# Kernel tuning notes

Measured on AMD Instinct MI355X. Metric: run time of the kernel, lower is better.

Reference implementation:

```python
import jax, jax.numpy as jnp
import numpy as np

E = 512      # embed_size
H = 8        # heads
HD = E // H  # head_dim
TN = 288     # time_num
FE = 4       # forward_expansion
N, T = 64, 512


def layernorm(x, g, b, eps=1e-5):
    mu = jnp.mean(x, axis=-1, keepdims=True)
    var = jnp.mean((x - mu) ** 2, axis=-1, keepdims=True)
    return (x - mu) * jax.lax.rsqrt(var + eps) * g + b


def setup_inputs() -> dict:
    key = jax.random.key(0)
    ks = jax.random.split(key, 12)
    w = lambda k, sh: jax.random.normal(k, sh, dtype=jnp.float32) * 0.02
    return {
        "value": jax.random.normal(ks[0], (N, T, E), dtype=jnp.float32),
        "key_in": jax.random.normal(ks[1], (N, T, E), dtype=jnp.float32),
        "query": jax.random.normal(ks[2], (N, T, E), dtype=jnp.float32),
        "i": 37,
        # One_hot_encoder params: learned identity-init table + linear to embed
        "I_mat": jnp.eye(TN, dtype=jnp.float32),
        "oh_W": w(ks[3], (TN, E)), "oh_b": jnp.zeros((E,), jnp.float32),
        # per-head projections (shared across heads, as in the torch module)
        "Wv": w(ks[4], (HD, HD)), "Wk": w(ks[5], (HD, HD)), "Wq": w(ks[6], (HD, HD)),
        "Wo": w(ks[7], (E, E)), "bo": jnp.zeros((E,), jnp.float32),
        "g1": jnp.ones((E,), jnp.float32), "b1": jnp.zeros((E,), jnp.float32),
        "g2": jnp.ones((E,), jnp.float32), "b2": jnp.zeros((E,), jnp.float32),
        "W1": w(ks[8], (E, FE * E)), "bf1": jnp.zeros((FE * E,), jnp.float32),
        "W2": w(ks[9], (FE * E, E)), "bf2": jnp.zeros((E,), jnp.float32),
    }


def reference(value, key_in, query, i, I_mat, oh_W, oh_b, Wv, Wk, Wq, Wo, bo,
              g1, b1, g2, b2, W1, bf1, W2, bf2):
    n, t, c = query.shape
    # One_hot_encoder: rows i..i+T-1 (mod time_num) of learned table -> linear
    rows = (i + jnp.arange(t)) % TN
    onehot = I_mat[rows] @ oh_W + oh_b            # (T, E), broadcast over N
    q_in = query + onehot[None, :, :]
    # per-head projections
    v = value.reshape(n, t, H, HD) @ Wv           # (N,T,H,HD)
    k = key_in.reshape(n, t, H, HD) @ Wk
    qh = q_in.reshape(n, t, H, HD) @ Wq
    # attention (note: scale uses sqrt(embed_size), per original code)
    energy = jnp.einsum("nqhd,nkhd->nhqk", qh, k) / jnp.sqrt(jnp.float32(E))
    attn = jax.nn.softmax(energy, axis=-1)
    out = jnp.einsum("nhqk,nkhd->nqhd", attn, v).reshape(n, t, E)
    out = out @ Wo + bo
    # residual + LN + FFN + residual + LN (dropout=0 -> identity)
    x = layernorm(out + q_in, g1, b1)
    ff = jax.nn.relu(x @ W1 + bf1) @ W2 + bf2
    return layernorm(ff + x, g2, b2)
```

## Files before the change

### kernel.cpp

```cpp
#include <hip/hip_runtime.h>

typedef __attribute__((ext_vector_type(8))) short s16x8;
typedef __attribute__((ext_vector_type(4))) float f32x4;

#define TN 288

__device__ __forceinline__ unsigned short f2bf(float f) {
  union { float f; unsigned u; } v; v.f = f;
  unsigned r = v.u + 0x7fffu + ((v.u >> 16) & 1u);
  return (unsigned short)(r >> 16);
}
__device__ __forceinline__ float bf2f(unsigned short u) {
  union { float f; unsigned u; } v; v.u = ((unsigned)u) << 16;
  return v.f;
}
__device__ __forceinline__ unsigned lds_addr(const void* p) {
  return (unsigned)(unsigned long long)(const __attribute__((address_space(3))) char*)p;
}
__device__ __forceinline__ void async_copy16(unsigned short* lds, const unsigned short* g) {
  __builtin_amdgcn_global_load_lds(
      (const __attribute__((address_space(1))) unsigned int*)g,
      (__attribute__((address_space(3))) unsigned int*)lds, 16, 0, 0);
}

__device__ __forceinline__ void pack_body(const float* __restrict__ W,
    unsigned short* __restrict__ out, int N, long t) {
  int lr = (int)(t & 15);
  int lg = (int)((t >> 4) & 3);
  long g6 = t >> 6;
  int nt = N >> 4;
  int n16 = (int)(g6 % nt);
  int kb = (int)(g6 / nt) << 5;
  int k = kb + lg * 8;
  int col = n16 * 16 + lr;
  s16x8 v;
#pragma unroll
  for (int j = 0; j < 8; ++j) v[j] = (short)f2bf(W[(size_t)(k + j) * N + col]);
  *(s16x8*)(out + t * 8) = v;
}

__global__ __launch_bounds__(256) void prep_kernel(const int* __restrict__ pi,
    const float* __restrict__ I_mat, const float* __restrict__ ohW,
    const float* __restrict__ ohb, float* __restrict__ onehot,
    const float* __restrict__ Wv, const float* __restrict__ Wk,
    const float* __restrict__ Wq, unsigned short* __restrict__ Wv_b,
    unsigned short* __restrict__ Wk_b, unsigned short* __restrict__ Wq_b,
    const float* __restrict__ Wo, const float* __restrict__ W1,
    const float* __restrict__ W2, unsigned short* __restrict__ Wop,
    unsigned short* __restrict__ W1p, unsigned short* __restrict__ W2p) {
  int b = blockIdx.x, tid = threadIdx.x;
  if (b < 512) {
    int t = b;
    int r = (pi[0] + t) % TN;
    float acc0 = ohb[tid], acc1 = ohb[tid + 256];
    const float* Ir = I_mat + (size_t)r * TN;
    for (int j = 0; j < TN; ++j) {
      float iv = Ir[j];
      acc0 += iv * ohW[(size_t)j * 512 + tid];
      acc1 += iv * ohW[(size_t)j * 512 + tid + 256];
    }
    onehot[(size_t)t * 512 + tid] = acc0;
    onehot[(size_t)t * 512 + tid + 256] = acc1;
  } else if (b < 640) {
    pack_body(Wo, Wop, 512, (long)(b - 512) * 256 + tid);
  } else if (b < 1152) {
    pack_body(W1, W1p, 2048, (long)(b - 640) * 256 + tid);
  } else if (b < 1664) {
    pack_body(W2, W2p, 512, (long)(b - 1152) * 256 + tid);
  } else {
    int which = b - 1664;
    const float* src = which == 0 ? Wv : (which == 1 ? Wk : Wq);
    unsigned short* dst = which == 0 ? Wv_b : (which == 1 ? Wk_b : Wq_b);
    float sc = which == 2 ? 0.06375871424f : 1.f;
#pragma unroll
    for (int j = 0; j < 4; ++j) {
      int i = tid * 16 + j * 4;
      float4 f = *(const float4*)(src + i);
      unsigned lo = (unsigned)f2bf(f.x * sc) | ((unsigned)f2bf(f.y * sc) << 16);
      unsigned hi = (unsigned)f2bf(f.z * sc) | ((unsigned)f2bf(f.w * sc) << 16);
      *(uint2*)(dst + i) = make_uint2(lo, hi);
    }
  }
}

__global__ __launch_bounds__(256) void proj_all(
    const float* __restrict__ value, const float* __restrict__ key_in,
    const float* __restrict__ query, const unsigned short* __restrict__ Wv_b,
    const unsigned short* __restrict__ Wk_b, const unsigned short* __restrict__ Wq_b,
    const float* __restrict__ onehot, unsigned short* __restrict__ vT,
    unsigned short* __restrict__ k_p, unsigned short* __restrict__ q_p) {
  __shared__ unsigned short As[64][40];
  __shared__ unsigned short Bs[64][40];
  __shared__ unsigned short Cs[64][72];
  const int which = blockIdx.x >> 12;
  const int mb = blockIdx.x & 4095;
  const float* A = which == 0 ? value : (which == 1 ? key_in : query);
  const unsigned short* B = which == 0 ? Wv_b : (which == 1 ? Wk_b : Wq_b);
  unsigned short* C = which == 0 ? vT : (which == 1 ? k_p : q_p);
  const bool qin = (which == 2);
  const int m0 = mb * 64;
  const int tid = threadIdx.x, w = tid >> 6, l = tid & 63, lr = l & 15, lg = l >> 4;
  const int wr = (w >> 1) * 32, wc = (w & 1) * 32;
  const int aRow = (tid * 8) >> 5, aK = (tid * 8) & 31;
  const int bK = (tid * 8) >> 6, bCol = (tid * 8) & 63;
  f32x4 acc[2][2] = {};
  for (int kb = 0; kb < 64; kb += 32) {
    size_t fl = (size_t)(m0 + aRow) * 64 + kb + aK;
    float4 f0 = *(const float4*)(A + fl);
    float4 f1 = *(const float4*)(A + fl + 4);
    if (qin) {
      const float* oh = onehot + (fl & 262143);
      float4 o0 = *(const float4*)(oh);
      float4 o1 = *(const float4*)(oh + 4);
      f0.x += o0.x; f0.y += o0.y; f0.z += o0.z; f0.w += o0.w;
      f1.x += o1.x; f1.y += o1.y; f1.z += o1.z; f1.w += o1.w;
    }
    s16x8 av;
    av[0] = (short)f2bf(f0.x); av[1] = (short)f2bf(f0.y);
    av[2] = (short)f2bf(f0.z); av[3] = (short)f2bf(f0.w);
    av[4] = (short)f2bf(f1.x); av[5] = (short)f2bf(f1.y);
    av[6] = (short)f2bf(f1.z); av[7] = (short)f2bf(f1.w);
    *(s16x8*)&As[aRow][aK] = av;
    s16x8 bv = *(const s16x8*)(B + (size_t)(kb + bK) * 64 + bCol);
#pragma unroll
    for (int j = 0; j < 8; ++j) Bs[bCol + j][bK] = (unsigned short)bv[j];
    __syncthreads();
    s16x8 af0 = *(const s16x8*)&As[wr + lr][lg * 8];
    s16x8 af1 = *(const s16x8*)&As[wr + 16 + lr][lg * 8];
    s16x8 bf0 = *(const s16x8*)&Bs[wc + lr][lg * 8];
    s16x8 bf1 = *(const s16x8*)&Bs[wc + 16 + lr][lg * 8];
    acc[0][0] = __builtin_amdgcn_mfma_f32_16x16x32_bf16(af0, bf0, acc[0][0], 0, 0, 0);
    acc[0][1] = __builtin_amdgcn_mfma_f32_16x16x32_bf16(af0, bf1, acc[0][1], 0, 0, 0);
    acc[1][0] = __builtin_amdgcn_mfma_f32_16x16x32_bf16(af1, bf0, acc[1][0], 0, 0, 0);
    acc[1][1] = __builtin_amdgcn_mfma_f32_16x16x32_bf16(af1, bf1, acc[1][1], 0, 0, 0);
    __syncthreads();
  }
  if (which != 0) {
#pragma unroll
    for (int fi = 0; fi < 2; ++fi)
#pragma unroll
      for (int fj = 0; fj < 2; ++fj)
#pragma unroll
        for (int r = 0; r < 4; ++r) {
          int row = m0 + wr + fi * 16 + lg * 4 + r;
          int col = wc + fj * 16 + lr;
          C[(size_t)row * 64 + col] = f2bf(acc[fi][fj][r]);
        }
  } else {
#pragma unroll
    for (int fi = 0; fi < 2; ++fi)
#pragma unroll
      for (int fj = 0; fj < 2; ++fj)
#pragma unroll
        for (int r = 0; r < 4; ++r)
          Cs[wr + fi * 16 + lg * 4 + r][wc + fj * 16 + lr] = f2bf(acc[fi][fj][r]);
    __syncthreads();
    int nIdx = m0 >> 12, t0 = (m0 >> 3) & 511;
#pragma unroll
    for (int it = 0; it < 2; ++it) {
      int p = tid + it * 256;
      int hh = p >> 6, d = p & 63;
      s16x8 vv;
#pragma unroll
      for (int j = 0; j < 8; ++j) vv[j] = (short)Cs[j * 8 + hh][d];
      *(s16x8*)(C + (((size_t)(nIdx * 8 + hh) * 64 + d) << 9) + t0) = vv;
    }
  }
}

template<bool RELU, bool OUTBF, bool RES>
__global__ __launch_bounds__(256) void gemmF(
    const unsigned short* __restrict__ A, int lda,
    const unsigned short* __restrict__ Bp, int ldbp, int nOff,
    const float* __restrict__ bias, void* __restrict__ Cout,
    const unsigned short* __restrict__ resid, int ldc,
    int M, int K, int nby) {
  __shared__ unsigned short As[2][8192];
  const int tid = threadIdx.x, w = tid >> 6, l = tid & 63, lr = l & 15, lg = l >> 4;
  const int nwg = gridDim.x;
  const int bid = (blockIdx.x & 7) * (nwg >> 3) + (blockIdx.x >> 3);
  const int bx = bid / nby, by = bid % nby;
  const int m0 = bx * 128;
  const int wr = (w >> 1) * 64, wc = (w & 1) * 64;
  const int srow = tid >> 3, sc8 = tid & 7;
  const int gcol = (sc8 ^ (srow & 7)) * 8;
  const unsigned short* Ag = A + (size_t)(m0 + srow) * lda + gcol;
  const size_t ldaa = (size_t)32 * lda;
  const unsigned short* Bg = Bp +
      ((size_t)(nOff >> 4) + by * 8 + (wc >> 4)) * 512 + lg * 128 + lr * 8;
  const size_t bks = (size_t)ldbp * 512;

  f32x4 acc[4][4] = {};
  s16x8 b0[4], b1[4];

#pragma unroll
  for (int it = 0; it < 4; ++it)
    async_copy16(&As[0][(it * 256 + tid) * 8], Ag + it * ldaa);
#pragma unroll
  for (int fj = 0; fj < 4; ++fj) {
    b0[fj] = *(const s16x8*)(Bg + fj * 512);
    b1[fj] = *(const s16x8*)(Bg + bks + fj * 512);
  }
  __syncthreads();

  int buf = 0;
  for (int kb = 0; kb < K; kb += 64) {
    int kn = (kb + 64 < K) ? kb + 64 : 0;
#pragma unroll
    for (int it = 0; it < 4; ++it)
      async_copy16(&As[buf ^ 1][(it * 256 + tid) * 8], Ag + kn + it * ldaa);
    s16x8 b0n[4];
    {
      const unsigned short* p = Bg + ((size_t)(kn >> 5)) * bks;
#pragma unroll
      for (int fj = 0; fj < 4; ++fj) b0n[fj] = *(const s16x8*)(p + fj * 512);
    }
    {
      s16x8 af[4];
#pragma unroll
      for (int fi = 0; fi < 4; ++fi) {
        int row = wr + fi * 16 + lr;
        af[fi] = *(const s16x8*)&As[buf][row * 64 + ((lg ^ (row & 7)) * 8)];
      }
#pragma unroll
      for (int fi = 0; fi < 4; ++fi)
#pragma unroll
        for (int fj = 0; fj < 4; ++fj)
          acc[fi][fj] = __builtin_amdgcn_mfma_f32_16x16x32_bf16(af[fi], b0[fj], acc[fi][fj], 0, 0, 0);
    }
    s16x8 b1n[4];
    {
      const unsigned short* p = Bg + ((size_t)((kn + 32) >> 5)) * bks;
#pragma unroll
      for (int fj = 0; fj < 4; ++fj) b1n[fj] = *(const s16x8*)(p + fj * 512);
    }
    {
      s16x8 af[4];
#pragma unroll
      for (int fi = 0; fi < 4; ++fi) {
        int row = wr + fi * 16 + lr;
        af[fi] = *(const s16x8*)&As[buf][row * 64 + (((4 + lg) ^ (row & 7)) * 8)];
      }
#pragma unroll
      for (int fi = 0; fi < 4; ++fi)
#pragma unroll
        for (int fj = 0; fj < 4; ++fj)
          acc[fi][fj] = __builtin_amdgcn_mfma_f32_16x16x32_bf16(af[fi], b1[fj], acc[fi][fj], 0, 0, 0);
    }
    __syncthreads();
#pragma unroll
    for (int fj = 0; fj < 4; ++fj) { b0[fj] = b0n[fj]; b1[fj] = b1n[fj]; }
    buf ^= 1;
  }

#pragma unroll
  for (int fj = 0; fj < 4; ++fj) {
    int colL = by * 128 + wc + fj * 16 + lr;
    float bv = bias[nOff + colL];
#pragma unroll
    for (int fi = 0; fi < 4; ++fi)
#pragma unroll
      for (int r = 0; r < 4; ++r) {
        int row = m0 + wr + fi * 16 + lg * 4 + r;
        size_t ci = (size_t)row * ldc + colL;
        float v = acc[fi][fj][r] + bv;
        if (RES) v += bf2f(resid[ci]);
        if (RELU) v = fmaxf(v, 0.f);
        if (OUTBF) ((unsigned short*)Cout)[ci] = f2bf(v);
        else ((float*)Cout)[ci] = v;
      }
  }
}

__global__ __launch_bounds__(256, 2) void attn_kernel(
    const unsigned short* __restrict__ Qp, const unsigned short* __restrict__ Kp,
    const unsigned short* __restrict__ Vt, unsigned short* __restrict__ Out) {
  __shared__ unsigned short KS[128][72];
  __shared__ unsigned short P[4][16][132];
  const int bid = blockIdx.x;
  const int qh = bid >> 9, g = bid & 511, h = g & 7, n = g >> 3;
  const int tid = threadIdx.x, w = tid >> 6, l = tid & 63, lr = l & 15, lg = l >> 4;
  const int q0 = qh * 256;

  s16x8 qf[4][2];
#pragma unroll
  for (int rt = 0; rt < 4; ++rt) {
    const size_t qb = (((size_t)(n * 512 + q0 + w * 64 + rt * 16 + lr)) * 8 + h) * 64;
    qf[rt][0] = *(const s16x8*)(Qp + qb + lg * 8);
    qf[rt][1] = *(const s16x8*)(Qp + qb + 32 + lg * 8);
  }
  const unsigned short* Vb = Vt + ((size_t)(n * 8 + h)) * 32768 + (size_t)lr * 512 + lg * 8;

  f32x4 oacc[4][4] = {};
  float m[4][4], lsum[4][4];
#pragma unroll
  for (int rt = 0; rt < 4; ++rt)
#pragma unroll
    for (int r = 0; r < 4; ++r) { m[rt][r] = -1e30f; lsum[rt][r] = 0.f; }
  s16x8 vreg[16];

#pragma unroll
  for (int it = 0; it < 4; ++it) {
    int idx = tid + it * 256;
    int rr = idx >> 3, dd = (idx & 7) * 8;
    *(s16x8*)&KS[rr][dd] =
        *(const s16x8*)(Kp + (((size_t)(n * 512 + rr)) * 8 + h) * 64 + dd);
  }
#pragma unroll
  for (int ks = 0; ks < 4; ++ks)
#pragma unroll
    for (int fj = 0; fj < 4; ++fj)
      vreg[ks * 4 + fj] = *(const s16x8*)(Vb + fj * 8192 + ks * 32);
  __syncthreads();

  for (int c = 0; c < 4; ++c) {
    if (c) {
      __syncthreads();
#pragma unroll
      for (int it = 0; it < 4; ++it) {
        int idx = tid + it * 256;
        int rr = idx >> 3, dd = (idx & 7) * 8;
        *(s16x8*)&KS[rr][dd] =
            *(const s16x8*)(Kp + (((size_t)(n * 512 + c * 128 + rr)) * 8 + h) * 64 + dd);
      }
#pragma unroll
      for (int ks = 0; ks < 4; ++ks)
#pragma unroll
        for (int fj = 0; fj < 4; ++fj)
          vreg[ks * 4 + fj] = *(const s16x8*)(Vb + fj * 8192 + c * 128 + ks * 32);
      __syncthreads();
    }
#pragma unroll
    for (int rt = 0; rt < 4; ++rt) {
      f32x4 sacc[8];
      __builtin_amdgcn_s_setprio(1);
#pragma unroll
      for (int f = 0; f < 8; ++f) {
        s16x8 b0 = *(const s16x8*)&KS[f * 16 + lr][lg * 8];
        s16x8 b1 = *(const s16x8*)&KS[f * 16 + lr][32 + lg * 8];
        f32x4 a = {};
        a = __builtin_amdgcn_mfma_f32_16x16x32_bf16(qf[rt][0], b0, a, 0, 0, 0);
        a = __builtin_amdgcn_mfma_f32_16x16x32_bf16(qf[rt][1], b1, a, 0, 0, 0);
        sacc[f] = a;
      }
      __builtin_amdgcn_s_setprio(0);

      float fs[4];
#pragma unroll
      for (int r = 0; r < 4; ++r) {
        float cm = sacc[0][r];
#pragma unroll
        for (int f = 1; f < 8; ++f) cm = fmaxf(cm, sacc[f][r]);
#pragma unroll
        for (int mk = 1; mk < 16; mk <<= 1) cm = fmaxf(cm, __shfl_xor(cm, mk));
        float mn = fmaxf(m[rt][r], cm);
        fs[r] = __builtin_amdgcn_exp2f(m[rt][r] - mn);
        m[rt][r] = mn;
        unsigned pa = lds_addr(&P[w][lg * 4 + r][lr]);
        float cs = 0.f;
#pragma unroll
        for (int f = 0; f < 8; ++f) {
          float p = __builtin_amdgcn_exp2f(sacc[f][r] - mn);
          asm volatile("ds_write_b16_d16_hi %0, %1 offset:%2"
                       :: "v"(pa), "v"(p), "i"(f * 32) : "memory");
          cs += p;
        }
#pragma unroll
        for (int mk = 1; mk < 16; mk <<= 1) cs += __shfl_xor(cs, mk);
        lsum[rt][r] = lsum[rt][r] * fs[r] + cs;
      }
#pragma unroll
      for (int fj = 0; fj < 4; ++fj)
#pragma unroll
        for (int r = 0; r < 4; ++r) oacc[rt][fj][r] *= fs[r];

      asm volatile("s_waitcnt lgkmcnt(0)" ::: "memory");
      __builtin_amdgcn_sched_barrier(0);
      __builtin_amdgcn_s_setprio(1);
#pragma unroll
      for (int ks = 0; ks < 4; ++ks) {
        s16x8 pa = *(const s16x8*)&P[w][lr][ks * 32 + lg * 8];
#pragma unroll
        for (int fj = 0; fj < 4; ++fj)
          oacc[rt][fj] = __builtin_amdgcn_mfma_f32_16x16x32_bf16(pa, vreg[ks * 4 + fj], oacc[rt][fj], 0, 0, 0);
      }
      __builtin_amdgcn_s_setprio(0);
    }
  }

#pragma unroll
  for (int rt = 0; rt < 4; ++rt)
#pragma unroll
    for (int fj = 0; fj < 4; ++fj)
#pragma unroll
      for (int r = 0; r < 4; ++r) {
        int qrow = q0 + w * 64 + rt * 16 + lg * 4 + r;
        Out[((size_t)(n * 512 + qrow)) * 512 + h * 64 + fj * 16 + lr] =
            f2bf(oacc[rt][fj][r] / lsum[rt][r]);
      }
}

template<bool XBF, bool RES, bool RBF, bool QIN, bool OUTBF>
__global__ __launch_bounds__(256) void ln_kernel(const void* __restrict__ Xv,
    const void* __restrict__ Rv, const float* __restrict__ onehot,
    const float* __restrict__ g, const float* __restrict__ bb,
    void* __restrict__ outv) {
  int row = blockIdx.x * 4 + (threadIdx.x >> 6);
  int l = threadIdx.x & 63;
  size_t base = (size_t)row * 512 + l * 8;
  float v[8];
  if (XBF) {
    s16x8 xv = *(const s16x8*)((const unsigned short*)Xv + base);
#pragma unroll
    for (int j = 0; j < 8; ++j) v[j] = bf2f((unsigned short)xv[j]);
  } else {
    const float* X = (const float*)Xv;
    float4 x0 = *(const float4*)(X + base);
    float4 x1 = *(const float4*)(X + base + 4);
    v[0] = x0.x; v[1] = x0.y; v[2] = x0.z; v[3] = x0.w;
    v[4] = x1.x; v[5] = x1.y; v[6] = x1.z; v[7] = x1.w;
  }
  if (RES) {
    if (RBF) {
      s16x8 rv = *(const s16x8*)((const unsigned short*)Rv + base);
#pragma unroll
      for (int j = 0; j < 8; ++j) v[j] += bf2f((unsigned short)rv[j]);
    } else {
      const float* R = (const float*)Rv;
      float4 r0 = *(const float4*)(R + base);
      float4 r1 = *(const float4*)(R + base + 4);
      v[0] += r0.x; v[1] += r0.y; v[2] += r0.z; v[3] += r0.w;
      v[4] += r1.x; v[5] += r1.y; v[6] += r1.z; v[7] += r1.w;
    }
  }
  if (QIN) {
    size_t ob = (size_t)(row & 511) * 512 + l * 8;
    float4 o0 = *(const float4*)(onehot + ob);
    float4 o1 = *(const float4*)(onehot + ob + 4);
    v[0] += o0.x; v[1] += o0.y; v[2] += o0.z; v[3] += o0.w;
    v[4] += o1.x; v[5] += o1.y; v[6] += o1.z; v[7] += o1.w;
  }
  float s = 0.f, ss = 0.f;
#pragma unroll
  for (int j = 0; j < 8; ++j) { s += v[j]; ss += v[j] * v[j]; }
#pragma unroll
  for (int mk = 1; mk < 64; mk <<= 1) { s += __shfl_xor(s, mk); ss += __shfl_xor(ss, mk); }
  float mu = s * (1.f / 512.f);
  float inv = rsqrtf(ss * (1.f / 512.f) - mu * mu + 1e-5f);
#pragma unroll
  for (int j = 0; j < 8; ++j) {
    int e = l * 8 + j;
    float y = (v[j] - mu) * inv * g[e] + bb[e];
    if (OUTBF) ((unsigned short*)outv)[base + j] = f2bf(y);
    else ((float*)outv)[base + j] = y;
  }
}

extern "C" void kernel_launch(void* const* d_in, const int* in_sizes, int n_in,
                              void* d_out, int out_size, void* d_ws, size_t ws_size,
                              hipStream_t stream) {
  const float* value  = (const float*)d_in[0];
  const float* key_in = (const float*)d_in[1];
  const float* query  = (const float*)d_in[2];
  const int*   pi     = (const int*)d_in[3];
  const float* I_mat  = (const float*)d_in[4];
  const float* ohW    = (const float*)d_in[5];
  const float* ohb    = (const float*)d_in[6];
  const float* Wv     = (const float*)d_in[7];
  const float* Wk     = (const float*)d_in[8];
  const float* Wq     = (const float*)d_in[9];
  const float* Wo     = (const float*)d_in[10];
  const float* bo     = (const float*)d_in[11];
  const float* g1     = (const float*)d_in[12];
  const float* b1     = (const float*)d_in[13];
  const float* g2     = (const float*)d_in[14];
  const float* b2     = (const float*)d_in[15];
  const float* W1     = (const float*)d_in[16];
  const float* bf1    = (const float*)d_in[17];
  const float* W2     = (const float*)d_in[18];
  const float* bf2    = (const float*)d_in[19];

  char* ws = (char*)d_ws;
  const size_t MB = 1024 * 1024;
  unsigned short* q_p  = (unsigned short*)d_out;
  unsigned short* k_p  = q_p + 16777216;
  unsigned short* vT     = (unsigned short*)(ws + 0);
  unsigned short* attn_o = (unsigned short*)(ws + 32 * MB);
  unsigned short* x_b    = (unsigned short*)(ws + 64 * MB);
  unsigned short* ff1h   = (unsigned short*)(ws + 0);
  float*          onehot = (float*)(ws + 96 * MB);
  unsigned short* Wv_b   = (unsigned short*)(ws + 97 * MB);
  unsigned short* Wk_b   = Wv_b + 4096;
  unsigned short* Wq_b   = Wk_b + 4096;
  unsigned short* Wop    = Wq_b + 4096;
  unsigned short* W1p    = Wop + 262144;
  unsigned short* W2p    = W1p + 1048576;

  prep_kernel<<<1667, 256, 0, stream>>>(pi, I_mat, ohW, ohb, onehot,
      Wv, Wk, Wq, Wv_b, Wk_b, Wq_b, Wo, W1, W2, Wop, W1p, W2p);

  proj_all<<<12288, 256, 0, stream>>>(value, key_in, query,
      Wv_b, Wk_b, Wq_b, onehot, vT, k_p, q_p);

  attn_kernel<<<1024, 256, 0, stream>>>(q_p, k_p, vT, attn_o);

  gemmF<false, true, false><<<1024, 256, 0, stream>>>(
      attn_o, 512, Wop, 32, 0, bo, x_b, nullptr, 512, 32768, 512, 4);
  ln_kernel<true, true, false, true, true><<<8192, 256, 0, stream>>>(
      x_b, query, onehot, g1, b1, x_b);

  for (int hf = 0; hf < 2; ++hf) {
    const unsigned short* xh = x_b + (size_t)hf * 16384 * 512;
    gemmF<true, true, false><<<2048, 256, 0, stream>>>(
        xh, 512, W1p, 128, 0, bf1, ff1h, nullptr, 2048, 16384, 512, 16);
    gemmF<false, false, true><<<512, 256, 0, stream>>>(
        ff1h, 2048, W2p, 32, 0, bf2, (float*)d_out + (size_t)hf * 16384 * 512,
        xh, 512, 16384, 2048, 4);
  }
  ln_kernel<false, false, false, false, false><<<8192, 256, 0, stream>>>(
      d_out, nullptr, nullptr, g2, b2, d_out);
}
```

Measured before the change: 460.5 us.

## Pre-swizzle V into MFMA fragment layout and halve attention query tile

The V projection now writes its output in a layout that matches the MFMA B-fragment order, so each lane can read its fragment with one contiguous 16-byte load. The attention kernel stops keeping all V fragments in registers; it loads them from global memory inside the PV loop, which is now kept rolled. Each block handles 128 queries instead of 256 and the grid doubles to 2048 blocks, which lowers register pressure and may raise occupancy. The cost is that K chunks are loaded and staged by twice as many blocks, and the V loads now sit on the critical path of the PV MFMAs.

```diff
diff --git a/kernel.cpp b/kernel.cpp
--- a/kernel.cpp
+++ b/kernel.cpp
@@ -87,7 +87,7 @@
     const float* __restrict__ value, const float* __restrict__ key_in,
     const float* __restrict__ query, const unsigned short* __restrict__ Wv_b,
     const unsigned short* __restrict__ Wk_b, const unsigned short* __restrict__ Wq_b,
-    const float* __restrict__ onehot, unsigned short* __restrict__ vT,
+    const float* __restrict__ onehot, unsigned short* __restrict__ vP,
     unsigned short* __restrict__ k_p, unsigned short* __restrict__ q_p) {
   __shared__ unsigned short As[64][40];
   __shared__ unsigned short Bs[64][40];
@@ -96,7 +96,7 @@
   const int mb = blockIdx.x & 4095;
   const float* A = which == 0 ? value : (which == 1 ? key_in : query);
   const unsigned short* B = which == 0 ? Wv_b : (which == 1 ? Wk_b : Wq_b);
-  unsigned short* C = which == 0 ? vT : (which == 1 ? k_p : q_p);
+  unsigned short* C = which == 0 ? vP : (which == 1 ? k_p : q_p);
   const bool qin = (which == 2);
   const int m0 = mb * 64;
   const int tid = threadIdx.x, w = tid >> 6, l = tid & 63, lr = l & 15, lg = l >> 4;
@@ -156,6 +156,7 @@
           Cs[wr + fi * 16 + lg * 4 + r][wc + fj * 16 + lr] = f2bf(acc[fi][fj][r]);
     __syncthreads();
     int nIdx = m0 >> 12, t0 = (m0 >> 3) & 511;
+    int cc = t0 >> 7, ksv = (t0 >> 5) & 3, lgv = (t0 >> 3) & 3;
 #pragma unroll
     for (int it = 0; it < 2; ++it) {
       int p = tid + it * 256;
@@ -163,7 +164,9 @@
       s16x8 vv;
 #pragma unroll
       for (int j = 0; j < 8; ++j) vv[j] = (short)Cs[j * 8 + hh][d];
-      *(s16x8*)(C + (((size_t)(nIdx * 8 + hh) * 64 + d) << 9) + t0) = vv;
+      size_t dst = ((size_t)(nIdx * 8 + hh)) * 32768 +
+                   (size_t)(((cc * 16 + ksv * 4 + (d >> 4)) * 64) + lgv * 16 + (d & 15)) * 8;
+      *(s16x8*)(C + dst) = vv;
     }
   }
 }
@@ -278,26 +281,25 @@
   __shared__ unsigned short KS[128][72];
   __shared__ unsigned short P[4][16][132];
   const int bid = blockIdx.x;
-  const int qh = bid >> 9, g = bid & 511, h = g & 7, n = g >> 3;
+  const int qq = bid >> 9, g = bid & 511, h = g & 7, n = g >> 3;
   const int tid = threadIdx.x, w = tid >> 6, l = tid & 63, lr = l & 15, lg = l >> 4;
-  const int q0 = qh * 256;
-
-  s16x8 qf[4][2];
-#pragma unroll
-  for (int rt = 0; rt < 4; ++rt) {
-    const size_t qb = (((size_t)(n * 512 + q0 + w * 64 + rt * 16 + lr)) * 8 + h) * 64;
+  const int q0 = qq * 128;
+
+  s16x8 qf[2][2];
+#pragma unroll
+  for (int rt = 0; rt < 2; ++rt) {
+    const size_t qb = (((size_t)(n * 512 + q0 + w * 32 + rt * 16 + lr)) * 8 + h) * 64;
     qf[rt][0] = *(const s16x8*)(Qp + qb + lg * 8);
     qf[rt][1] = *(const s16x8*)(Qp + qb + 32 + lg * 8);
   }
-  const unsigned short* Vb = Vt + ((size_t)(n * 8 + h)) * 32768 + (size_t)lr * 512 + lg * 8;
-
-  f32x4 oacc[4][4] = {};
-  float m[4][4], lsum[4][4];
-#pragma unroll
-  for (int rt = 0; rt < 4; ++rt)
+  const unsigned short* Vfb = Vt + ((size_t)(n * 8 + h)) * 32768 + (size_t)l * 8;
+
+  f32x4 oacc[2][4] = {};
+  float m[2][4], lsum[2][4];
+#pragma unroll
+  for (int rt = 0; rt < 2; ++rt)
 #pragma unroll
     for (int r = 0; r < 4; ++r) { m[rt][r] = -1e30f; lsum[rt][r] = 0.f; }
-  s16x8 vreg[16];
 
 #pragma unroll
   for (int it = 0; it < 4; ++it) {
@@ -306,11 +308,6 @@
     *(s16x8*)&KS[rr][dd] =
         *(const s16x8*)(Kp + (((size_t)(n * 512 + rr)) * 8 + h) * 64 + dd);
   }
-#pragma unroll
-  for (int ks = 0; ks < 4; ++ks)
-#pragma unroll
-    for (int fj = 0; fj < 4; ++fj)
-      vreg[ks * 4 + fj] = *(const s16x8*)(Vb + fj * 8192 + ks * 32);
   __syncthreads();
 
   for (int c = 0; c < 4; ++c) {
@@ -323,15 +320,11 @@
         *(s16x8*)&KS[rr][dd] =
             *(const s16x8*)(Kp + (((size_t)(n * 512 + c * 128 + rr)) * 8 + h) * 64 + dd);
       }
-#pragma unroll
-      for (int ks = 0; ks < 4; ++ks)
-#pragma unroll
-        for (int fj = 0; fj < 4; ++fj)
-          vreg[ks * 4 + fj] = *(const s16x8*)(Vb + fj * 8192 + c * 128 + ks * 32);
       __syncthreads();
     }
-#pragma unroll
-    for (int rt = 0; rt < 4; ++rt) {
+    const unsigned short* Vc = Vfb + ((size_t)(c * 16) << 9);
+#pragma unroll
+    for (int rt = 0; rt < 2; ++rt) {
       f32x4 sacc[8];
       __builtin_amdgcn_s_setprio(1);
 #pragma unroll
@@ -377,24 +370,29 @@
       asm volatile("s_waitcnt lgkmcnt(0)" ::: "memory");
       __builtin_amdgcn_sched_barrier(0);
       __builtin_amdgcn_s_setprio(1);
-#pragma unroll
+#pragma unroll 1
       for (int ks = 0; ks < 4; ++ks) {
+        s16x8 bv0 = *(const s16x8*)(Vc + ((ks * 4 + 0) << 9));
+        s16x8 bv1 = *(const s16x8*)(Vc + ((ks * 4 + 1) << 9));
+        s16x8 bv2 = *(const s16x8*)(Vc + ((ks * 4 + 2) << 9));
+        s16x8 bv3 = *(const s16x8*)(Vc + ((ks * 4 + 3) << 9));
         s16x8 pa = *(const s16x8*)&P[w][lr][ks * 32 + lg * 8];
-#pragma unroll
-        for (int fj = 0; fj < 4; ++fj)
-          oacc[rt][fj] = __builtin_amdgcn_mfma_f32_16x16x32_bf16(pa, vreg[ks * 4 + fj], oacc[rt][fj], 0, 0, 0);
+        oacc[rt][0] = __builtin_amdgcn_mfma_f32_16x16x32_bf16(pa, bv0, oacc[rt][0], 0, 0, 0);
+        oacc[rt][1] = __builtin_amdgcn_mfma_f32_16x16x32_bf16(pa, bv1, oacc[rt][1], 0, 0, 0);
+        oacc[rt][2] = __builtin_amdgcn_mfma_f32_16x16x32_bf16(pa, bv2, oacc[rt][2], 0, 0, 0);
+        oacc[rt][3] = __builtin_amdgcn_mfma_f32_16x16x32_bf16(pa, bv3, oacc[rt][3], 0, 0, 0);
       }
       __builtin_amdgcn_s_setprio(0);
     }
   }
 
 #pragma unroll
-  for (int rt = 0; rt < 4; ++rt)
+  for (int rt = 0; rt < 2; ++rt)
 #pragma unroll
     for (int fj = 0; fj < 4; ++fj)
 #pragma unroll
       for (int r = 0; r < 4; ++r) {
-        int qrow = q0 + w * 64 + rt * 16 + lg * 4 + r;
+        int qrow = q0 + w * 32 + rt * 16 + lg * 4 + r;
         Out[((size_t)(n * 512 + qrow)) * 512 + h * 64 + fj * 16 + lr] =
             f2bf(oacc[rt][fj][r] / lsum[rt][r]);
       }
@@ -484,7 +482,7 @@
   const size_t MB = 1024 * 1024;
   unsigned short* q_p  = (unsigned short*)d_out;
   unsigned short* k_p  = q_p + 16777216;
-  unsigned short* vT     = (unsigned short*)(ws + 0);
+  unsigned short* vP     = (unsigned short*)(ws + 0);
   unsigned short* attn_o = (unsigned short*)(ws + 32 * MB);
   unsigned short* x_b    = (unsigned short*)(ws + 64 * MB);
   unsigned short* ff1h   = (unsigned short*)(ws + 0);
@@ -500,9 +498,9 @@
       Wv, Wk, Wq, Wv_b, Wk_b, Wq_b, Wo, W1, W2, Wop, W1p, W2p);
 
   proj_all<<<12288, 256, 0, stream>>>(value, key_in, query,
-      Wv_b, Wk_b, Wq_b, onehot, vT, k_p, q_p);
-
-  attn_kernel<<<1024, 256, 0, stream>>>(q_p, k_p, vT, attn_o);
+      Wv_b, Wk_b, Wq_b, onehot, vP, k_p, q_p);
+
+  attn_kernel<<<2048, 256, 0, stream>>>(q_p, k_p, vP, attn_o);
 
   gemmF<false, true, false><<<1024, 256, 0, stream>>>(
       attn_o, 512, Wop, 32, 0, bo, x_b, nullptr, 512, 32768, 512, 4);
```

Result: faster. 441.1 us (-4.2%).
